# Kernel tuning notes

Hardware: AMD Instinct MI355X
Metric: run time of the kernel (lower is better)

The kernel has to match this reference:

```python
import jax, jax.numpy as jnp
import numpy as np

GRID = 16
PAD = 32
RADIUS = 8
SIGMA = 1.5
B = 8192
N_SEEDS = 24


def setup_inputs() -> dict:
    key = jax.random.key(0)
    k1, k2 = jax.random.split(key)
    # predicted seeds: (x, y, phase), coords in [0, GRID)
    output = jax.random.uniform(k1, (B, N_SEEDS * 3), dtype=jnp.float32) * GRID
    # target seeds: (x, y, amp), coords in [0, 2*GRID)
    targets = jax.random.uniform(k2, (B, N_SEEDS * 3), dtype=jnp.float32) * (2 * GRID)
    return {"output": output, "targets": targets}


def _forward(output, targets):
    Bn = output.shape[0]
    seeds = output.reshape(Bn, -1, 3)   # (B, N, 3): x, y, phase
    tgt = targets.reshape(Bn, -1, 3)    # (B, M, 3): x, y, amp

    # --- discrete Voronoi on GRID x GRID (vectorized over batch) ---
    c = jnp.arange(GRID, dtype=output.dtype)
    xx, yy = jnp.meshgrid(c, c, indexing='ij')  # (GRID, GRID)
    dist = jnp.sqrt((xx[None, :, :, None] - seeds[:, None, None, :, 0]) ** 2
                    + (yy[None, :, :, None] - seeds[:, None, None, :, 1]) ** 2)
    labels = jnp.argmin(dist, axis=-1)  # (B, GRID, GRID) int

    # circular support on the inner grid (np.ogrid[-r:r, -r:r] convention)
    cc = jnp.arange(-RADIUS, RADIUS)
    inner = (cc[:, None] ** 2 + cc[None, :] ** 2) <= RADIUS ** 2
    labels = jnp.where(inner[None], labels, 0)

    # zero-pad voronoi labels to PAD x PAD
    pw = (PAD - GRID) // 2
    padded = jnp.pad(labels, ((0, 0), (pw, pw), (pw, pw)))  # (B, PAD, PAD)

    # --- gather phase per pixel, zero outside circle on padded grid ---
    phases = seeds[:, :, 2]  # (B, N)
    phase = jnp.take_along_axis(phases, padded.reshape(Bn, -1), axis=1).reshape(Bn, PAD, PAD)
    pc = jnp.arange(PAD)
    center = PAD // 2
    outside = (pc[:, None] - center) ** 2 + (pc[None, :] - center) ** 2 > RADIUS ** 2
    phase = jnp.where(outside[None], jnp.zeros_like(phase), phase)

    # --- density = amp(=1) * exp(i * 2*pi * phase), shifted FFT magnitude ---
    two_pi = 2.0 * jnp.pi
    density = jax.lax.complex(jnp.cos(two_pi * phase), jnp.sin(two_pi * phase))
    pred = jnp.fft.fftshift(density, axes=(-2, -1))
    pred = jnp.fft.fft2(pred)
    pred_dp = jnp.abs(jnp.fft.fftshift(pred, axes=(-2, -1)))  # (B, PAD, PAD)

    # --- target diffraction: sum of Gaussians on (2*GRID)x(2*GRID) grid ---
    xc = jnp.arange(PAD, dtype=targets.dtype)  # height == width == 2*GRID == PAD
    tx = tgt[:, :, 0][:, :, None, None]
    ty = tgt[:, :, 1][:, :, None, None]
    amp = tgt[:, :, 2][:, :, None, None]
    # torch: x varies along last axis, y along second-to-last
    d2 = (xc[None, None, None, :] - tx) ** 2 + (xc[None, None, :, None] - ty) ** 2
    tgt_dp = jnp.sum(amp * jnp.exp(-d2 / (2.0 * SIGMA ** 2)), axis=1)  # (B, PAD, PAD)

    # --- chi-square (global max-normalization and reductions) ---
    p = pred_dp / jnp.max(pred_dp)
    t = tgt_dp / jnp.max(tgt_dp)
    return jnp.sum((p - t) ** 2) / jnp.sqrt(jnp.sum(p ** 2) * jnp.sum(t ** 2))


def reference(output, targets):
    return _forward(output, targets)
```

## Files before the change

### kernel.cpp

```cpp
#include <hip/hip_runtime.h>
#include <math.h>

#define NS 24

typedef float v2f __attribute__((ext_vector_type(2)));
typedef float v4f __attribute__((ext_vector_type(4)));


struct PixTab { unsigned short v[196]; };
__device__ constexpr PixTab make_pix() {
    PixTab t{};
    int n = 0;
    const int w[16] = {0,3,5,6,6,7,7,7,8,7,7,7,6,6,5,3};
    for (int yy = 0; yy < 16; ++yy)
        for (int x = 16 - w[yy]; x <= 16 + w[yy]; ++x)
            if (x < 24) { t.v[n] = (unsigned short)((yy << 8) | x); n = n + 1; }
    t.v[195] = (unsigned short)((8 << 8) | 24);
    return t;
}
__device__ constexpr PixTab PIX = make_pix();

constexpr float twc_(int p) {
    const float C[17] = {
        1.0f, 0.98078528040323044913f, 0.92387953251128675613f, 0.83146961230254523708f,
        0.70710678118654752440f, 0.55557023301960222474f, 0.38268343236508977173f,
        0.19509032201612826785f, 0.0f,
        -0.19509032201612826785f, -0.38268343236508977173f, -0.55557023301960222474f,
        -0.70710678118654752440f, -0.83146961230254523708f, -0.92387953251128675613f,
        -0.98078528040323044913f, -1.0f };
    return (p <= 16) ? C[p] : C[32 - p];
}
constexpr float tws_(int p) {
    const float S[17] = {
        0.0f, 0.19509032201612826785f, 0.38268343236508977173f, 0.55557023301960222474f,
        0.70710678118654752440f, 0.83146961230254523708f, 0.92387953251128675613f,
        0.98078528040323044913f, 1.0f,
        0.98078528040323044913f, 0.92387953251128675613f, 0.83146961230254523708f,
        0.70710678118654752440f, 0.55557023301960222474f, 0.38268343236508977173f,
        0.19509032201612826785f, 0.0f };
    return (p <= 16) ? -S[p] : S[32 - p];
}
struct alignas(16) TW1T { float v[8 * 18 * 2]; };
__device__ constexpr TW1T make_tw1() {
    TW1T t{};
    for (int l0 = 0; l0 < 8; ++l0)
        for (int xi = 0; xi < 17; ++xi) {
            int p = (l0 * (xi + 8)) & 31;
            t.v[(l0 * 18 + xi) * 2 + 0] = twc_(p);
            t.v[(l0 * 18 + xi) * 2 + 1] = tws_(p);
        }
    return t;
}
__device__ constexpr TW1T TW1G = make_tw1();
struct alignas(16) TW2T { float v[4 * 18 * 2]; };
__device__ constexpr TW2T make_tw2() {
    TW2T t{};
    for (int k0 = 0; k0 < 4; ++k0)
        for (int yp = 0; yp < 16; ++yp) {
            int p = (k0 * (yp + 8)) & 31;
            t.v[(k0 * 18 + yp) * 2 + 0] = twc_(p);
            t.v[(k0 * 18 + yp) * 2 + 1] = tws_(p);
        }
    return t;
}
__device__ constexpr TW2T TW2G = make_tw2();

static __device__ __forceinline__ v2f cmul(v2f e, v2f w) {
    v2f m = (v2f){e.y, e.y} * (v2f){w.y, w.x};
    return __builtin_elementwise_fma((v2f){e.x, e.x}, w, (v2f){-m.x, m.y});
}
static __device__ __forceinline__ float mag(v2f h) {
    v2f q = h * h;
    return sqrtf(q.x + q.y);
}

template <int CTRL>
static __device__ __forceinline__ float dpp_step(float x) {
    int y = __builtin_amdgcn_update_dpp(0, __float_as_int(x), CTRL, 0xf, 0xf, true);
    return __int_as_float(y);
}
static __device__ __forceinline__ float wave_sum(float x) {
    x += dpp_step<0x111>(x);
    x += dpp_step<0x112>(x);
    x += dpp_step<0x114>(x);
    x += dpp_step<0x118>(x);
    x += dpp_step<0x142>(x);
    x += dpp_step<0x143>(x);
    return x;
}
static __device__ __forceinline__ float wave_max(float x) {
    x = fmaxf(x, dpp_step<0x111>(x));
    x = fmaxf(x, dpp_step<0x112>(x));
    x = fmaxf(x, dpp_step<0x114>(x));
    x = fmaxf(x, dpp_step<0x118>(x));
    x = fmaxf(x, dpp_step<0x142>(x));
    x = fmaxf(x, dpp_step<0x143>(x));
    return x;
}

__global__ __launch_bounds__(256)
void loss_main(const float* __restrict__ output, const float* __restrict__ targets,
               float* __restrict__ partials, int B) {
    __shared__ float tx[NS], ty[NS], ta[NS];
    __shared__ float2 e24s;
    __shared__ __align__(16) float gx[NS * 32];
    __shared__ __align__(16) float gyT[32 * 24];
    __shared__ __align__(16) float e2f[16 * 18 * 2];
    __shared__ __align__(16) float tw2f[4 * 36];
    __shared__ __align__(16) float gT2f[32 * 36];
    __shared__ __align__(16) char uA[5120];
    __shared__ float redm[4][5];

    float* tw1f = (float*)uA;
    float* pmf  = (float*)uA;

    const int b = blockIdx.x;
    const int t = threadIdx.x;
    const float* so = output + b * NS * 3;
    const float* tg = targets + b * NS * 3;

    if (t == 0) {
        float sv0, cv0;
        __sincosf(6.2831853071795864f * so[2], &sv0, &cv0);
        e24s = make_float2(cv0 - 1.0f, sv0);
    }
    if (t >= 64 && t < 64 + NS) {
        int s = t - 64;
        tx[s] = tg[3 * s + 0];
        ty[s] = tg[3 * s + 1];
        ta[s] = tg[3 * s + 2];
    }
    if (t < 108) {
        if (t < 72) *(v4f*)&tw1f[t * 4] = *(const v4f*)&TW1G.v[t * 4];
        else        *(v4f*)&tw2f[(t - 72) * 4] = *(const v4f*)&TW2G.v[(t - 72) * 4];
    }
    for (int i = t; i < 16 * 18; i += 256) *(v2f*)&e2f[i * 2] = (v2f){0.f, 0.f};
    __syncthreads();

    for (int idx = t; idx < NS * 32; idx += 256) {
        int s = idx >> 5, c = idx & 31;
        float dx = (float)c - tx[s];
        gx[idx] = ta[s] * __expf(dx * dx * (-1.0f / 4.5f));
    }
    for (int idx = t; idx < 32 * 24; idx += 256) {
        int r = idx / 24, s = idx - r * 24;
        float dy = (float)r - ty[s];
        gyT[idx] = __expf(dy * dy * (-1.0f / 4.5f));
    }

    if (t < 196) {
        int pv = (int)PIX.v[t];
        int yy = pv >> 8, x = pv & 255;
        float ph;
        if (t < 195) {
            float fi = (float)yy, fj = (float)(x - 8);
            float bd = 1e30f, bph = 0.0f;
#pragma unroll
            for (int s = 0; s < NS; ++s) {
                float ddx = fi - so[3 * s + 0];
                float ddy = fj - so[3 * s + 1];
                float d2 = __builtin_fmaf(ddx, ddx, ddy * ddy);
                bool cle = d2 < bd;
                bd  = cle ? d2 : bd;
                bph = cle ? so[3 * s + 2] : bph;
            }
            ph = bph;
        } else {
            ph = so[2];
        }
        float sv_, cv_;
        __sincosf(6.2831853071795864f * ph, &sv_, &cv_);
        *(v2f*)&e2f[(yy * 18 + (x - 8)) * 2] = (v2f){cv_ - 1.0f, sv_};
    }
    __syncthreads();

    if (t < 128) {
        int yy = t >> 3, l0 = t & 7;
        const float* row = &e2f[yy * 36];
        const float* twr = &tw1f[l0 * 36];
        v2f c0 = {0,0}, c1 = {0,0}, c2 = {0,0}, c3 = {0,0};
#pragma unroll
        for (int q = 0; q < 8; ++q) {
            v4f e4 = *(const v4f*)&row[q * 4];
            v4f w4 = *(const v4f*)&twr[q * 4];
            v2f ca = cmul((v2f){e4.x, e4.y}, (v2f){w4.x, w4.y});
            v2f cb = cmul((v2f){e4.z, e4.w}, (v2f){w4.z, w4.w});
            if ((q & 1) == 0) { c0 += ca; c1 += cb; }
            else              { c2 += ca; c3 += cb; }
        }
        {
            v2f e16 = *(const v2f*)&row[32];
            v2f w16 = *(const v2f*)&twr[32];
            c0 += cmul(e16, w16);
        }
        v2f a = c0 + c2, bb = c0 - c2;
        v2f cc = c1 + c3, d = c1 - c3;
        v2f du = {d.y, -d.x};
        *(v2f*)&gT2f[l0 * 36 + yy * 2]        = a + cc;
        *(v2f*)&gT2f[(l0 + 8) * 36 + yy * 2]  = bb + du;
        *(v2f*)&gT2f[(l0 + 16) * 36 + yy * 2] = a - cc;
        *(v2f*)&gT2f[(l0 + 24) * 36 + yy * 2] = bb - du;
    }
    __syncthreads();

    if (t < 128) {
        int l = t >> 2, k0 = t & 3;
        const float* gTr = &gT2f[l * 36];
        const float* twr = &tw2f[k0 * 36];
        v2f c[8];
#pragma unroll
        for (int q = 0; q < 4; ++q) {
            v4f glo = *(const v4f*)&gTr[q * 4];
            v4f ghi = *(const v4f*)&gTr[q * 4 + 16];
            v4f wlo = *(const v4f*)&twr[q * 4];
            v4f whi = *(const v4f*)&twr[q * 4 + 16];
            c[2 * q]     = cmul((v2f){glo.x, glo.y}, (v2f){wlo.x, wlo.y})
                         + cmul((v2f){ghi.x, ghi.y}, (v2f){whi.x, whi.y});
            c[2 * q + 1] = cmul((v2f){glo.z, glo.w}, (v2f){wlo.z, wlo.w})
                         + cmul((v2f){ghi.z, ghi.w}, (v2f){whi.z, whi.w});
        }
        v2f Ea = c[0] + c[4], Eb = c[0] - c[4];
        v2f Ec = c[2] + c[6], Ed = c[2] - c[6];
        v2f Edu = {Ed.y, -Ed.x};
        v2f E0 = Ea + Ec, E1 = Eb + Edu, E2 = Ea - Ec, E3 = Eb - Edu;
        v2f Oa = c[1] + c[5], Ob = c[1] - c[5];
        v2f Oc = c[3] + c[7], Od = c[3] - c[7];
        v2f Odu = {Od.y, -Od.x};
        v2f O0 = Oa + Oc, O1 = Ob + Odu, O2 = Oa - Oc, O3 = Ob - Odu;
        const float s2 = 0.70710678118654752440f;
        v2f w1O = (v2f){s2, s2} * (v2f){O1.x + O1.y, O1.y - O1.x};
        v2f w3O = (v2f){s2, s2} * (v2f){O3.y - O3.x, -(O3.x + O3.y)};
        v2f miO = {O2.y, -O2.x};
        {
            float2 e24 = e24s;
            float ar2 = (k0 == 0) ? 1.f : (k0 == 2) ? -1.f : 0.f;
            float ai2 = (k0 == 1) ? 1.f : (k0 == 3) ? -1.f : 0.f;
            float sgn = (l & 1) ? -1.f : 1.f;
            v2f T = {sgn * (e24.x * ar2 - e24.y * ai2),
                     sgn * (e24.x * ai2 + e24.y * ar2)};
            E0 += T; E1 += T; E2 += T; E3 += T;
        }
        v2f h0 = E0 + O0;
        if (t == 0) h0.x += 1024.0f;
        int v = (l + 16) & 31;
        pmf[(k0 + 16) * 40 + v] = mag(h0);
        pmf[(k0 + 20) * 40 + v] = mag(E1 + w1O);
        pmf[(k0 + 24) * 40 + v] = mag(E2 + miO);
        pmf[(k0 + 28) * 40 + v] = mag(E3 + w3O);
        pmf[(k0)      * 40 + v] = mag(E0 - O0);
        pmf[(k0 + 4)  * 40 + v] = mag(E1 - w1O);
        pmf[(k0 + 8)  * 40 + v] = mag(E2 - miO);
        pmf[(k0 + 12) * 40 + v] = mag(E3 - w3O);
    }
    __syncthreads();

    float mp = 0.f, mt = 0.f, sp2 = 0.f, st2 = 0.f, spt = 0.f;
    if (t < 128) {
        int r = t >> 3;
        int c0i = (t & 7) * 4;
        v4f p4a = *(const v4f*)&pmf[r * 40 + c0i];
        v4f p4b = *(const v4f*)&pmf[(r + 16) * 40 + c0i];
        v2f a01 = {0,0}, a23 = {0,0}, b01 = {0,0}, b23 = {0,0};
#pragma unroll
        for (int q = 0; q < 6; ++q) {
            v4f gy4a = *(const v4f*)&gyT[r * 24 + q * 4];
            v4f gy4b = *(const v4f*)&gyT[(r + 16) * 24 + q * 4];
#pragma unroll
            for (int j = 0; j < 4; ++j) {
                int s = 4 * q + j;
                v4f g4 = *(const v4f*)&gx[s * 32 + c0i];
                float ga = (j == 0) ? gy4a.x : (j == 1) ? gy4a.y : (j == 2) ? gy4a.z : gy4a.w;
                float gb = (j == 0) ? gy4b.x : (j == 1) ? gy4b.y : (j == 2) ? gy4b.z : gy4b.w;
                a01 = __builtin_elementwise_fma((v2f){ga, ga}, (v2f){g4.x, g4.y}, a01);
                a23 = __builtin_elementwise_fma((v2f){ga, ga}, (v2f){g4.z, g4.w}, a23);
                b01 = __builtin_elementwise_fma((v2f){gb, gb}, (v2f){g4.x, g4.y}, b01);
                b23 = __builtin_elementwise_fma((v2f){gb, gb}, (v2f){g4.z, g4.w}, b23);
            }
        }
        v2f pa01 = {p4a.x, p4a.y}, pa23 = {p4a.z, p4a.w};
        v2f pb01 = {p4b.x, p4b.y}, pb23 = {p4b.z, p4b.w};
        v2f s2v = pa01 * pa01 + pa23 * pa23 + pb01 * pb01 + pb23 * pb23;
        v2f t2v = a01 * a01 + a23 * a23 + b01 * b01 + b23 * b23;
        v2f ptv = pa01 * a01 + pa23 * a23 + pb01 * b01 + pb23 * b23;
        sp2 = s2v.x + s2v.y;
        st2 = t2v.x + t2v.y;
        spt = ptv.x + ptv.y;
        mp = fmaxf(fmaxf(fmaxf(p4a.x, p4a.y), fmaxf(p4a.z, p4a.w)),
                   fmaxf(fmaxf(p4b.x, p4b.y), fmaxf(p4b.z, p4b.w)));
        v2f tm = __builtin_elementwise_max(__builtin_elementwise_max(a01, a23),
                                           __builtin_elementwise_max(b01, b23));
        mt = fmaxf(tm.x, tm.y);
    }

    sp2 = wave_sum(sp2);
    st2 = wave_sum(st2);
    spt = wave_sum(spt);
    mp  = wave_max(mp);
    mt  = wave_max(mt);
    int wave = t >> 6, lane = t & 63;
    if (lane == 63) {
        redm[wave][0] = sp2; redm[wave][1] = st2; redm[wave][2] = spt;
        redm[wave][3] = mp;  redm[wave][4] = mt;
    }
    __syncthreads();
    if (t == 0) {
        sp2 = redm[0][0] + redm[1][0] + redm[2][0] + redm[3][0];
        st2 = redm[0][1] + redm[1][1] + redm[2][1] + redm[3][1];
        spt = redm[0][2] + redm[1][2] + redm[2][2] + redm[3][2];
        mp = fmaxf(fmaxf(redm[0][3], redm[1][3]), fmaxf(redm[2][3], redm[3][3]));
        mt = fmaxf(fmaxf(redm[0][4], redm[1][4]), fmaxf(redm[2][4], redm[3][4]));
        partials[0 * B + b] = sp2;
        partials[1 * B + b] = st2;
        partials[2 * B + b] = spt;
        partials[3 * B + b] = mp;
        partials[4 * B + b] = mt;
    }
}

__global__ __launch_bounds__(1024)
void finalize_loss(const float* __restrict__ partials, float* __restrict__ out, int B) {
    __shared__ double reds[16][3];
    __shared__ float redx[16][2];
    const int t = threadIdx.x;
    double sp2 = 0.0, st2 = 0.0, spt = 0.0;
    float mp = 0.f, mt = 0.f;
    for (int i = t; i < B; i += 1024) {
        sp2 += (double)partials[0 * B + i];
        st2 += (double)partials[1 * B + i];
        spt += (double)partials[2 * B + i];
        mp = fmaxf(mp, partials[3 * B + i]);
        mt = fmaxf(mt, partials[4 * B + i]);
    }
    for (int off = 32; off > 0; off >>= 1) {
        sp2 += __shfl_down(sp2, off);
        st2 += __shfl_down(st2, off);
        spt += __shfl_down(spt, off);
        mp = fmaxf(mp, __shfl_down(mp, off));
        mt = fmaxf(mt, __shfl_down(mt, off));
    }
    int wave = t >> 6, lane = t & 63;
    if (lane == 0) {
        reds[wave][0] = sp2; reds[wave][1] = st2; reds[wave][2] = spt;
        redx[wave][0] = mp;  redx[wave][1] = mt;
    }
    __syncthreads();
    if (t == 0) {
        for (int w = 1; w < 16; ++w) {
            sp2 += reds[w][0];
            st2 += reds[w][1];
            spt += reds[w][2];
            mp = fmaxf(mp, redx[w][0]);
            mt = fmaxf(mt, redx[w][1]);
        }
        double Mp = (double)mp, Mt = (double)mt;
        double loss = (sp2 * (Mt / Mp) + st2 * (Mp / Mt) - 2.0 * spt) / sqrt(sp2 * st2);
        out[0] = (float)loss;
    }
}

extern "C" void kernel_launch(void* const* d_in, const int* in_sizes, int n_in,
                              void* d_out, int out_size, void* d_ws, size_t ws_size,
                              hipStream_t stream) {
    const float* output  = (const float*)d_in[0];
    const float* targets = (const float*)d_in[1];
    int B = in_sizes[0] / (NS * 3);
    float* partials = (float*)d_ws;

    loss_main<<<B, 256, 0, stream>>>(output, targets, partials, B);
    finalize_loss<<<1, 1024, 0, stream>>>(partials, (float*)d_out, B);
}
```

Baseline: 97.04 us.

## Cut barriers: read targets directly, single-wave reduction, two pixels per thread

Drops the shared staging of target seeds and the separate zero-fill pass, removing one block barrier; zeros are now written only to non-circle cells, using a constexpr index table. The Voronoi search handles two pixels per thread with packed float2 math. The final target-Gaussian sum and reduction run on a single wave with four rows per thread, which removes the cross-wave shared reduction and its barrier. The cost is less parallelism in the last stage, and more repeated global loads of target values inside the Gaussian loops.

Result: no change. 97.81 us (+0.8%).

```diff
diff --git a/kernel.cpp b/kernel.cpp
--- a/kernel.cpp
+++ b/kernel.cpp
@@ -20,6 +20,23 @@
 }
 __device__ constexpr PixTab PIX = make_pix();
 
+struct ZTab { unsigned short v[76]; };
+__device__ constexpr ZTab make_ztab() {
+    ZTab z{};
+    bool mark[16][17] = {};
+    const int w[16] = {0,3,5,6,6,7,7,7,8,7,7,7,6,6,5,3};
+    for (int yy = 0; yy < 16; ++yy)
+        for (int x = 16 - w[yy]; x <= 16 + w[yy]; ++x)
+            if (x < 24) mark[yy][x - 8] = true;
+    mark[8][16] = true;
+    int n = 0;
+    for (int yy = 0; yy < 16; ++yy)
+        for (int xi = 0; xi < 17; ++xi)
+            if (!mark[yy][xi]) { z.v[n] = (unsigned short)(yy * 18 + xi); n = n + 1; }
+    return z;
+}
+__device__ constexpr ZTab ZT = make_ztab();
+
 constexpr float twc_(int p) {
     const float C[17] = {
         1.0f, 0.98078528040323044913f, 0.92387953251128675613f, 0.83146961230254523708f,
@@ -101,7 +118,6 @@
 __global__ __launch_bounds__(256)
 void loss_main(const float* __restrict__ output, const float* __restrict__ targets,
                float* __restrict__ partials, int B) {
-    __shared__ float tx[NS], ty[NS], ta[NS];
     __shared__ float2 e24s;
     __shared__ __align__(16) float gx[NS * 32];
     __shared__ __align__(16) float gyT[32 * 24];
@@ -109,7 +125,6 @@
     __shared__ __align__(16) float tw2f[4 * 36];
     __shared__ __align__(16) float gT2f[32 * 36];
     __shared__ __align__(16) char uA[5120];
-    __shared__ float redm[4][5];
 
     float* tw1f = (float*)uA;
     float* pmf  = (float*)uA;
@@ -124,53 +139,46 @@
         __sincosf(6.2831853071795864f * so[2], &sv0, &cv0);
         e24s = make_float2(cv0 - 1.0f, sv0);
     }
-    if (t >= 64 && t < 64 + NS) {
-        int s = t - 64;
-        tx[s] = tg[3 * s + 0];
-        ty[s] = tg[3 * s + 1];
-        ta[s] = tg[3 * s + 2];
-    }
     if (t < 108) {
         if (t < 72) *(v4f*)&tw1f[t * 4] = *(const v4f*)&TW1G.v[t * 4];
         else        *(v4f*)&tw2f[(t - 72) * 4] = *(const v4f*)&TW2G.v[(t - 72) * 4];
     }
-    for (int i = t; i < 16 * 18; i += 256) *(v2f*)&e2f[i * 2] = (v2f){0.f, 0.f};
-    __syncthreads();
-
     for (int idx = t; idx < NS * 32; idx += 256) {
         int s = idx >> 5, c = idx & 31;
-        float dx = (float)c - tx[s];
-        gx[idx] = ta[s] * __expf(dx * dx * (-1.0f / 4.5f));
+        float dx = (float)c - tg[3 * s];
+        gx[idx] = tg[3 * s + 2] * __expf(dx * dx * (-1.0f / 4.5f));
     }
     for (int idx = t; idx < 32 * 24; idx += 256) {
         int r = idx / 24, s = idx - r * 24;
-        float dy = (float)r - ty[s];
+        float dy = (float)r - tg[3 * s + 1];
         gyT[idx] = __expf(dy * dy * (-1.0f / 4.5f));
     }
-
-    if (t < 196) {
-        int pv = (int)PIX.v[t];
-        int yy = pv >> 8, x = pv & 255;
-        float ph;
-        if (t < 195) {
-            float fi = (float)yy, fj = (float)(x - 8);
-            float bd = 1e30f, bph = 0.0f;
-#pragma unroll
-            for (int s = 0; s < NS; ++s) {
-                float ddx = fi - so[3 * s + 0];
-                float ddy = fj - so[3 * s + 1];
-                float d2 = __builtin_fmaf(ddx, ddx, ddy * ddy);
-                bool cle = d2 < bd;
-                bd  = cle ? d2 : bd;
-                bph = cle ? so[3 * s + 2] : bph;
-            }
-            ph = bph;
-        } else {
-            ph = so[2];
-        }
-        float sv_, cv_;
-        __sincosf(6.2831853071795864f * ph, &sv_, &cv_);
-        *(v2f*)&e2f[(yy * 18 + (x - 8)) * 2] = (v2f){cv_ - 1.0f, sv_};
+    if (t < 98) {
+        int pv0 = PIX.v[t], pv1 = PIX.v[t + 98];
+        int yy0 = pv0 >> 8, x0 = (pv0 & 255) - 8;
+        int yy1 = pv1 >> 8, x1 = (pv1 & 255) - 8;
+        v2f FI = {(float)yy0, (float)yy1};
+        v2f FJ = {(float)x0, (float)x1};
+        v2f bd = {1e30f, 1e30f};
+        v2f bph = {0.f, 0.f};
+#pragma unroll
+        for (int s = 0; s < NS; ++s) {
+            float sx = so[3 * s], sy = so[3 * s + 1], phs = so[3 * s + 2];
+            v2f dX = FI - (v2f){sx, sx};
+            v2f dY = FJ - (v2f){sy, sy};
+            v2f d2 = __builtin_elementwise_fma(dX, dX, dY * dY);
+            if (d2.x < bd.x) { bd.x = d2.x; bph.x = phs; }
+            if (d2.y < bd.y) { bd.y = d2.y; bph.y = phs; }
+        }
+        float ph1 = (t == 97) ? so[2] : bph.y;
+        float sv0, cv0, sv1, cv1;
+        __sincosf(6.2831853071795864f * bph.x, &sv0, &cv0);
+        __sincosf(6.2831853071795864f * ph1, &sv1, &cv1);
+        *(v2f*)&e2f[(yy0 * 18 + x0) * 2] = (v2f){cv0 - 1.0f, sv0};
+        *(v2f*)&e2f[(yy1 * 18 + x1) * 2] = (v2f){cv1 - 1.0f, sv1};
+    } else if (t < 98 + 76) {
+        int idx = (int)ZT.v[t - 98];
+        *(v2f*)&e2f[idx * 2] = (v2f){0.f, 0.f};
     }
     __syncthreads();
 
@@ -254,66 +262,62 @@
     }
     __syncthreads();
 
-    float mp = 0.f, mt = 0.f, sp2 = 0.f, st2 = 0.f, spt = 0.f;
-    if (t < 128) {
-        int r = t >> 3;
+    if (t < 64) {
+        int rr = t >> 3;
         int c0i = (t & 7) * 4;
-        v4f p4a = *(const v4f*)&pmf[r * 40 + c0i];
-        v4f p4b = *(const v4f*)&pmf[(r + 16) * 40 + c0i];
-        v2f a01 = {0,0}, a23 = {0,0}, b01 = {0,0}, b23 = {0,0};
+        v2f a01[4] = {{0,0},{0,0},{0,0},{0,0}};
+        v2f a23[4] = {{0,0},{0,0},{0,0},{0,0}};
 #pragma unroll
         for (int q = 0; q < 6; ++q) {
-            v4f gy4a = *(const v4f*)&gyT[r * 24 + q * 4];
-            v4f gy4b = *(const v4f*)&gyT[(r + 16) * 24 + q * 4];
+            v4f gy0 = *(const v4f*)&gyT[rr * 24 + q * 4];
+            v4f gy1 = *(const v4f*)&gyT[(rr + 8) * 24 + q * 4];
+            v4f gy2 = *(const v4f*)&gyT[(rr + 16) * 24 + q * 4];
+            v4f gy3 = *(const v4f*)&gyT[(rr + 24) * 24 + q * 4];
 #pragma unroll
             for (int j = 0; j < 4; ++j) {
-                int s = 4 * q + j;
-                v4f g4 = *(const v4f*)&gx[s * 32 + c0i];
-                float ga = (j == 0) ? gy4a.x : (j == 1) ? gy4a.y : (j == 2) ? gy4a.z : gy4a.w;
-                float gb = (j == 0) ? gy4b.x : (j == 1) ? gy4b.y : (j == 2) ? gy4b.z : gy4b.w;
-                a01 = __builtin_elementwise_fma((v2f){ga, ga}, (v2f){g4.x, g4.y}, a01);
-                a23 = __builtin_elementwise_fma((v2f){ga, ga}, (v2f){g4.z, g4.w}, a23);
-                b01 = __builtin_elementwise_fma((v2f){gb, gb}, (v2f){g4.x, g4.y}, b01);
-                b23 = __builtin_elementwise_fma((v2f){gb, gb}, (v2f){g4.z, g4.w}, b23);
+                v4f g4 = *(const v4f*)&gx[(4 * q + j) * 32 + c0i];
+                float g0 = (j == 0) ? gy0.x : (j == 1) ? gy0.y : (j == 2) ? gy0.z : gy0.w;
+                float g1 = (j == 0) ? gy1.x : (j == 1) ? gy1.y : (j == 2) ? gy1.z : gy1.w;
+                float g2 = (j == 0) ? gy2.x : (j == 1) ? gy2.y : (j == 2) ? gy2.z : gy2.w;
+                float g3 = (j == 0) ? gy3.x : (j == 1) ? gy3.y : (j == 2) ? gy3.z : gy3.w;
+                v2f glo = {g4.x, g4.y}, ghi = {g4.z, g4.w};
+                a01[0] = __builtin_elementwise_fma((v2f){g0, g0}, glo, a01[0]);
+                a23[0] = __builtin_elementwise_fma((v2f){g0, g0}, ghi, a23[0]);
+                a01[1] = __builtin_elementwise_fma((v2f){g1, g1}, glo, a01[1]);
+                a23[1] = __builtin_elementwise_fma((v2f){g1, g1}, ghi, a23[1]);
+                a01[2] = __builtin_elementwise_fma((v2f){g2, g2}, glo, a01[2]);
+                a23[2] = __builtin_elementwise_fma((v2f){g2, g2}, ghi, a23[2]);
+                a01[3] = __builtin_elementwise_fma((v2f){g3, g3}, glo, a01[3]);
+                a23[3] = __builtin_elementwise_fma((v2f){g3, g3}, ghi, a23[3]);
             }
         }
-        v2f pa01 = {p4a.x, p4a.y}, pa23 = {p4a.z, p4a.w};
-        v2f pb01 = {p4b.x, p4b.y}, pb23 = {p4b.z, p4b.w};
-        v2f s2v = pa01 * pa01 + pa23 * pa23 + pb01 * pb01 + pb23 * pb23;
-        v2f t2v = a01 * a01 + a23 * a23 + b01 * b01 + b23 * b23;
-        v2f ptv = pa01 * a01 + pa23 * a23 + pb01 * b01 + pb23 * b23;
-        sp2 = s2v.x + s2v.y;
-        st2 = t2v.x + t2v.y;
-        spt = ptv.x + ptv.y;
-        mp = fmaxf(fmaxf(fmaxf(p4a.x, p4a.y), fmaxf(p4a.z, p4a.w)),
-                   fmaxf(fmaxf(p4b.x, p4b.y), fmaxf(p4b.z, p4b.w)));
-        v2f tm = __builtin_elementwise_max(__builtin_elementwise_max(a01, a23),
-                                           __builtin_elementwise_max(b01, b23));
-        mt = fmaxf(tm.x, tm.y);
-    }
-
-    sp2 = wave_sum(sp2);
-    st2 = wave_sum(st2);
-    spt = wave_sum(spt);
-    mp  = wave_max(mp);
-    mt  = wave_max(mt);
-    int wave = t >> 6, lane = t & 63;
-    if (lane == 63) {
-        redm[wave][0] = sp2; redm[wave][1] = st2; redm[wave][2] = spt;
-        redm[wave][3] = mp;  redm[wave][4] = mt;
-    }
-    __syncthreads();
-    if (t == 0) {
-        sp2 = redm[0][0] + redm[1][0] + redm[2][0] + redm[3][0];
-        st2 = redm[0][1] + redm[1][1] + redm[2][1] + redm[3][1];
-        spt = redm[0][2] + redm[1][2] + redm[2][2] + redm[3][2];
-        mp = fmaxf(fmaxf(redm[0][3], redm[1][3]), fmaxf(redm[2][3], redm[3][3]));
-        mt = fmaxf(fmaxf(redm[0][4], redm[1][4]), fmaxf(redm[2][4], redm[3][4]));
-        partials[0 * B + b] = sp2;
-        partials[1 * B + b] = st2;
-        partials[2 * B + b] = spt;
-        partials[3 * B + b] = mp;
-        partials[4 * B + b] = mt;
+        float sp2 = 0.f, st2 = 0.f, spt = 0.f, mp = 0.f, mt = 0.f;
+#pragma unroll
+        for (int k = 0; k < 4; ++k) {
+            v4f p4 = *(const v4f*)&pmf[(rr + 8 * k) * 40 + c0i];
+            v2f p01 = {p4.x, p4.y}, p23 = {p4.z, p4.w};
+            v2f s2v = __builtin_elementwise_fma(p23, p23, p01 * p01);
+            v2f t2v = __builtin_elementwise_fma(a23[k], a23[k], a01[k] * a01[k]);
+            v2f ptv = __builtin_elementwise_fma(p23, a23[k], p01 * a01[k]);
+            sp2 += s2v.x + s2v.y;
+            st2 += t2v.x + t2v.y;
+            spt += ptv.x + ptv.y;
+            mp = fmaxf(mp, fmaxf(fmaxf(p4.x, p4.y), fmaxf(p4.z, p4.w)));
+            v2f tm = __builtin_elementwise_max(a01[k], a23[k]);
+            mt = fmaxf(mt, fmaxf(tm.x, tm.y));
+        }
+        sp2 = wave_sum(sp2);
+        st2 = wave_sum(st2);
+        spt = wave_sum(spt);
+        mp  = wave_max(mp);
+        mt  = wave_max(mt);
+        if (t == 63) {
+            partials[0 * B + b] = sp2;
+            partials[1 * B + b] = st2;
+            partials[2 * B + b] = spt;
+            partials[3 * B + b] = mp;
+            partials[4 * B + b] = mt;
+        }
     }
 }
 
```
